# Performance work log

Hardware: AMD Instinct MI355X
Metric: run time of the kernel (lower is better)

## Reference

```python
import jax, jax.numpy as jnp
import numpy as np

B, N, F, H, MH = 8, 1024, 768, 12, 3072
DH = F // H
EPS = 1e-5

def _ln(x, g, b):
    mu = jnp.mean(x, axis=-1, keepdims=True)
    var = jnp.mean(jnp.square(x - mu), axis=-1, keepdims=True)
    return (x - mu) * jax.lax.rsqrt(var + EPS) * g + b

def setup_inputs() -> dict:
    key = jax.random.key(0)
    ks = jax.random.split(key, 16)
    s = 1.0 / np.sqrt(F)
    sm = 1.0 / np.sqrt(MH)
    return {
        "x": jax.random.normal(ks[0], (B, N, F), dtype=jnp.float32),
        "Wq": jax.random.uniform(ks[1], (F, F), jnp.float32, -s, s),
        "bq": jax.random.uniform(ks[2], (F,), jnp.float32, -s, s),
        "Wk": jax.random.uniform(ks[3], (F, F), jnp.float32, -s, s),
        "bk": jax.random.uniform(ks[4], (F,), jnp.float32, -s, s),
        "Wv": jax.random.uniform(ks[5], (F, F), jnp.float32, -s, s),
        "bv": jax.random.uniform(ks[6], (F,), jnp.float32, -s, s),
        "Wo": jax.random.uniform(ks[7], (F, F), jnp.float32, -s, s),
        "bo": jax.random.uniform(ks[8], (F,), jnp.float32, -s, s),
        "ln1_g": jnp.ones((F,), jnp.float32),
        "ln1_b": jnp.zeros((F,), jnp.float32),
        "ln2_g": jnp.ones((F,), jnp.float32),
        "ln2_b": jnp.zeros((F,), jnp.float32),
        "W1": jax.random.uniform(ks[9], (F, MH), jnp.float32, -s, s),
        "b1": jax.random.uniform(ks[10], (MH,), jnp.float32, -s, s),
        "W2": jax.random.uniform(ks[11], (MH, F), jnp.float32, -sm, sm),
        "b2": jax.random.uniform(ks[12], (F,), jnp.float32, -sm, sm),
    }

def reference(x, Wq, bq, Wk, bk, Wv, bv, Wo, bo, ln1_g, ln1_b, ln2_g, ln2_b, W1, b1, W2, b2):
    xn = _ln(x, ln1_g, ln1_b)
    # low-rank (here full-rank, rank=-1) QKV projections, split into heads -> [b,h,n,dh]
    q = (xn @ Wq + bq).reshape(B, N, H, DH).transpose(0, 2, 1, 3)
    k = (xn @ Wk + bk).reshape(B, N, H, DH).transpose(0, 2, 1, 3)
    v = (xn @ Wv + bv).reshape(B, N, H, DH).transpose(0, 2, 1, 3)
    # note: original scales by sqrt(feats), NOT sqrt(d_head)
    score = jax.nn.softmax(jnp.einsum('bhif,bhjf->bhij', q, k) / jnp.sqrt(jnp.float32(F)), axis=-1)
    attn = jnp.einsum('bhij,bhjf->bhif', score, v)
    attn = attn.transpose(0, 2, 1, 3).reshape(B, N, F)
    out = (attn @ Wo + bo) + x  # dropout p=0.0
    h = _ln(out, ln2_g, ln2_b)
    h = jax.nn.gelu(h @ W1 + b1, approximate=False)
    h = jax.nn.gelu(h @ W2 + b2, approximate=False)  # second GELU per source
    return h + out
```

## Files before the change

### kernel.cpp

```cpp
#include <hip/hip_runtime.h>
#include <math.h>

#define B_ 8
#define N_ 1024
#define F_ 768
#define H_ 12
#define DH_ 64
#define MH_ 3072
#define MROWS (B_ * N_)

typedef unsigned short u16;
typedef unsigned int u32;
typedef __bf16 bf16x8 __attribute__((ext_vector_type(8)));
typedef float f32x4 __attribute__((ext_vector_type(4)));

__device__ inline f32x4 mfma16(bf16x8 a, bf16x8 b, f32x4 c) {
  return __builtin_amdgcn_mfma_f32_16x16x32_bf16(a, b, c, 0, 0, 0);
}

__device__ inline u16 f2bu(float f) {
  u32 b = __builtin_bit_cast(u32, f);
  b += 0x7fffu + ((b >> 16) & 1u);
  return (u16)(b >> 16);
}
__device__ inline float bu2f(u16 u) {
  u32 x = ((u32)u) << 16;
  return __builtin_bit_cast(float, x);
}
__device__ inline float gelu_exact(float x) {
  return 0.5f * x * (1.0f + erff(x * 0.70710678118654752f));
}

#define AS1 __attribute__((address_space(1)))
#define AS3 __attribute__((address_space(3)))
__device__ inline void glds16(const void* g, void* l) {
  __builtin_amdgcn_global_load_lds((const AS1 void*)g, (AS3 void*)l, 16, 0, 0);
}

__device__ inline float ldf(const float* p) { return *p; }
__device__ inline float ldf(const u16* p) { return bu2f(*p); }

template <typename Tin>
__global__ __launch_bounds__(256) void transpose_bf16(
    const Tin* __restrict__ in, u16* __restrict__ out, int R, int C) {
  __shared__ float tile[64][65];
  size_t ibase = (size_t)blockIdx.z * (size_t)R * (size_t)C;
  size_t obase = (size_t)blockIdx.z * (size_t)R * (size_t)C;
  int r0 = blockIdx.y << 6, c0 = blockIdx.x << 6;
  int t = threadIdx.x;
#pragma unroll
  for (int i = 0; i < 16; ++i) {
    int idx = t + (i << 8);
    int r = idx >> 6, c = idx & 63;
    tile[r][c] = ldf(&in[ibase + (size_t)(r0 + r) * C + (c0 + c)]);
  }
  __syncthreads();
#pragma unroll
  for (int i = 0; i < 16; ++i) {
    int idx = t + (i << 8);
    int rr = idx >> 6, cc = idx & 63;
    out[obase + (size_t)(c0 + rr) * R + (r0 + cc)] = f2bu(tile[cc][rr]);
  }
}

__global__ __launch_bounds__(256) void concat_bias(
    const float* __restrict__ a, const float* __restrict__ b,
    const float* __restrict__ c, float* __restrict__ o) {
  int i = blockIdx.x * 256 + threadIdx.x;
  if (i < 768) o[i] = a[i];
  else if (i < 1536) o[i] = b[i - 768];
  else o[i] = c[i - 1536];
}

__global__ __launch_bounds__(256) void ln_to_bf16(
    const float* __restrict__ X, const float* __restrict__ gw,
    const float* __restrict__ bw, u16* __restrict__ Y) {
  int row = blockIdx.x;
  int t = threadIdx.x;
  const float* xr = X + (size_t)row * F_;
  float v0 = xr[t], v1 = xr[t + 256], v2 = xr[t + 512];
  float s = v0 + v1 + v2;
  float ss = v0 * v0 + v1 * v1 + v2 * v2;
#pragma unroll
  for (int off = 1; off < 64; off <<= 1) {
    s += __shfl_xor(s, off, 64);
    ss += __shfl_xor(ss, off, 64);
  }
  __shared__ float red[8];
  int wid = t >> 6, lane = t & 63;
  if (lane == 0) { red[wid] = s; red[4 + wid] = ss; }
  __syncthreads();
  s = red[0] + red[1] + red[2] + red[3];
  ss = red[4] + red[5] + red[6] + red[7];
  float mu = s * (1.0f / F_);
  float var = ss * (1.0f / F_) - mu * mu;
  float rstd = rsqrtf(var + 1e-5f);
  u16* yr = Y + (size_t)row * F_;
  yr[t] = f2bu((v0 - mu) * rstd * gw[t] + bw[t]);
  yr[t + 256] = f2bu((v1 - mu) * rstd * gw[t + 256] + bw[t + 256]);
  yr[t + 512] = f2bu((v2 - mu) * rstd * gw[t + 512] + bw[t + 512]);
}

template <int MODE>
__global__ __launch_bounds__(256) void gemm_bt(
    const u16* __restrict__ A, const u16* __restrict__ Bt,
    const float* __restrict__ bias, void* __restrict__ outp,
    const float* __restrict__ resid, int Ndim, int Kdim, float qscale) {
  __shared__ __attribute__((aligned(16))) u16 As[2][128][32];
  __shared__ __attribute__((aligned(16))) u16 Bs[2][128][32];
  int t = threadIdx.x;
  int lane = t & 63, wid = t >> 6;

  int nwg = gridDim.x;
  int q8 = nwg >> 3;
  int bid = blockIdx.x;
  int swz = (bid & 7) * q8 + (bid >> 3);
  int nnt = Ndim >> 7;
  int mt = swz / nnt, nt = swz - mt * nnt;
  int row0 = mt << 7, col0 = nt << 7;

  int wr = (wid >> 1) << 6, wc = (wid & 1) << 6;
  int lr = lane & 15, lk = (lane >> 4) << 3;
  int rbase = (lane >> 4) << 2;
  f32x4 zero = {0.f, 0.f, 0.f, 0.f};
  f32x4 acc[4][4];
#pragma unroll
  for (int m = 0; m < 4; ++m)
#pragma unroll
    for (int n = 0; n < 4; ++n) acc[m][n] = zero;

  int o0 = (wid << 10) + (lane << 4);
  int srow = o0 >> 6;
  int scol = (o0 & 63) >> 1;
  const u16* Ag = A + (size_t)(row0 + srow) * Kdim + scol;
  const u16* Bg = Bt + (size_t)(col0 + srow) * Kdim + scol;
  char* AsB = (char*)&As[0][0][0] + (wid << 10);
  char* BsB = (char*)&Bs[0][0][0] + (wid << 10);
  size_t half = (size_t)64 * Kdim;

  auto STAGE = [&](int buf, int kt) {
    int bo = buf << 13;
    glds16(Ag + kt, AsB + bo);
    glds16(Ag + kt + half, AsB + bo + 4096);
    glds16(Bg + kt, BsB + bo);
    glds16(Bg + kt + half, BsB + bo + 4096);
  };

  STAGE(0, 0);
  __syncthreads();
  int nk = Kdim >> 5;
  for (int ki = 0; ki < nk; ++ki) {
    int buf = ki & 1;
    if (ki + 1 < nk) STAGE(buf ^ 1, (ki + 1) << 5);
    bf16x8 af[4], bfr[4];
#pragma unroll
    for (int m = 0; m < 4; ++m) af[m] = *(const bf16x8*)&As[buf][wr + (m << 4) + lr][lk];
#pragma unroll
    for (int n = 0; n < 4; ++n) bfr[n] = *(const bf16x8*)&Bs[buf][wc + (n << 4) + lr][lk];
#pragma unroll
    for (int m = 0; m < 4; ++m)
#pragma unroll
      for (int n = 0; n < 4; ++n) acc[m][n] = mfma16(af[m], bfr[n], acc[m][n]);
    __syncthreads();
  }

#pragma unroll
  for (int n = 0; n < 4; ++n) {
    int col = col0 + wc + (n << 4) + lr;
    float bc = bias[col];
    int sub = 0, hh = 0, dh = 0;
    float sc = 1.0f;
    if constexpr (MODE == 0) {
      sub = (col >= 1536) ? 2 : (col >= 768 ? 1 : 0);
      int c = col - sub * 768;
      hh = c >> 6; dh = c & 63;
      sc = (sub == 0) ? qscale : 1.0f;
    }
#pragma unroll
    for (int m = 0; m < 4; ++m) {
#pragma unroll
      for (int r = 0; r < 4; ++r) {
        int row = row0 + wr + (m << 4) + rbase + r;
        float val = acc[m][n][r] + bc;
        if constexpr (MODE == 0) {
          int b = row >> 10, nn = row & 1023;
          ((u16*)outp)[(size_t)sub * 6291456 +
                       ((((size_t)b * H_ + hh) << 10) + nn) * DH_ + dh] = f2bu(val * sc);
        } else if constexpr (MODE == 1) {
          val += resid[(size_t)row * Ndim + col];
          ((float*)outp)[(size_t)row * Ndim + col] = val;
        } else if constexpr (MODE == 2) {
          ((u16*)outp)[(size_t)row * Ndim + col] = f2bu(gelu_exact(val));
        } else {
          val = gelu_exact(val) + resid[(size_t)row * Ndim + col];
          ((float*)outp)[(size_t)row * Ndim + col] = val;
        }
      }
    }
  }
}

__global__ __launch_bounds__(256, 3) void attn_fwd(
    const u16* __restrict__ Q, const u16* __restrict__ K,
    const u16* __restrict__ Vt, u16* __restrict__ Aout) {
  __shared__ __attribute__((aligned(16))) u16 Ks[64][72];
  __shared__ __attribute__((aligned(16))) u16 Vs[64][72];
  __shared__ __attribute__((aligned(16))) u16 Ps[4][32][72];
  int t = threadIdx.x, lane = t & 63, wid = t >> 6;

  int bid = blockIdx.x;
  int swz = (bid & 7) * 96 + (bid >> 3);
  int bh = swz >> 3;
  int qt = swz & 7;
  int q0 = (qt << 7) + (wid << 5);

  int lr = lane & 15, lk = (lane >> 4) << 3;
  int rbase = (lane >> 4) << 2;

  bf16x8 qf[2][2];
#pragma unroll
  for (int m = 0; m < 2; ++m)
#pragma unroll
    for (int ks = 0; ks < 2; ++ks)
      qf[m][ks] = *(const bf16x8*)&Q[((size_t)bh * N_ + q0 + (m << 4) + lr) * DH_ + (ks << 5) + lk];

  float lsum[2][4];
  f32x4 zero = {0.f, 0.f, 0.f, 0.f};
  f32x4 Oacc[2][4];
#pragma unroll
  for (int m = 0; m < 2; ++m) {
#pragma unroll
    for (int r = 0; r < 4; ++r) lsum[m][r] = 0.f;
#pragma unroll
    for (int nd = 0; nd < 4; ++nd) Oacc[m][nd] = zero;
  }

  int srow = t >> 3;
  int scol = (t & 7) << 3;
  const u16* Kg = K + ((size_t)bh * N_ + srow) * DH_ + scol;
  const u16* Vg = Vt + ((size_t)bh * DH_ + srow) * N_ + scol;

  for (int kt = 0; kt < 16; ++kt) {
    __syncthreads();
    *(uint4*)&Ks[srow][scol]      = *(const uint4*)(Kg + (size_t)(kt << 6) * DH_);
    *(uint4*)&Ks[srow + 32][scol] = *(const uint4*)(Kg + (size_t)((kt << 6) + 32) * DH_);
    *(uint4*)&Vs[srow][scol]      = *(const uint4*)(Vg + (kt << 6));
    *(uint4*)&Vs[srow + 32][scol] = *(const uint4*)(Vg + (size_t)32 * N_ + (kt << 6));
    __syncthreads();

    f32x4 s[2][4];
#pragma unroll
    for (int m = 0; m < 2; ++m)
#pragma unroll
      for (int n = 0; n < 4; ++n) s[m][n] = zero;
#pragma unroll
    for (int ks = 0; ks < 2; ++ks) {
      bf16x8 kf[4];
#pragma unroll
      for (int n = 0; n < 4; ++n) kf[n] = *(const bf16x8*)&Ks[(n << 4) + lr][(ks << 5) + lk];
#pragma unroll
      for (int m = 0; m < 2; ++m)
#pragma unroll
        for (int n = 0; n < 4; ++n) s[m][n] = mfma16(qf[m][ks], kf[n], s[m][n]);
    }

#pragma unroll
    for (int m = 0; m < 2; ++m)
#pragma unroll
      for (int n = 0; n < 4; ++n)
#pragma unroll
        for (int r = 0; r < 4; ++r) {
          float p = exp2f(s[m][n][r]);
          lsum[m][r] += p;
          Ps[wid][(m << 4) + rbase + r][(n << 4) + lr] = f2bu(p);
        }

#pragma unroll
    for (int ks = 0; ks < 2; ++ks) {
      bf16x8 pf[2], vf[4];
#pragma unroll
      for (int m = 0; m < 2; ++m) pf[m] = *(const bf16x8*)&Ps[wid][(m << 4) + lr][(ks << 5) + lk];
#pragma unroll
      for (int nd = 0; nd < 4; ++nd) vf[nd] = *(const bf16x8*)&Vs[(nd << 4) + lr][(ks << 5) + lk];
#pragma unroll
      for (int m = 0; m < 2; ++m)
#pragma unroll
        for (int nd = 0; nd < 4; ++nd) Oacc[m][nd] = mfma16(pf[m], vf[nd], Oacc[m][nd]);
    }
  }

  int b = bh / H_, h = bh % H_;
#pragma unroll
  for (int m = 0; m < 2; ++m)
#pragma unroll
    for (int r = 0; r < 4; ++r) {
      float sv = lsum[m][r];
#pragma unroll
      for (int off = 1; off < 16; off <<= 1) sv += __shfl_xor(sv, off, 64);
      float inv = 1.0f / sv;
      int row = q0 + (m << 4) + rbase + r;
      size_t orow = ((size_t)b * N_ + row) * F_ + (size_t)h * DH_;
#pragma unroll
      for (int nd = 0; nd < 4; ++nd)
        Aout[orow + (nd << 4) + lr] = f2bu(Oacc[m][nd][r] * inv);
    }
}

extern "C" void kernel_launch(void* const* d_in, const int* in_sizes, int n_in,
                              void* d_out, int out_size, void* d_ws, size_t ws_size,
                              hipStream_t stream) {
  (void)in_sizes; (void)n_in; (void)out_size; (void)ws_size;
  const float* x   = (const float*)d_in[0];
  const float* Wq  = (const float*)d_in[1];
  const float* bq  = (const float*)d_in[2];
  const float* Wk  = (const float*)d_in[3];
  const float* bk  = (const float*)d_in[4];
  const float* Wv  = (const float*)d_in[5];
  const float* bv  = (const float*)d_in[6];
  const float* Wo  = (const float*)d_in[7];
  const float* bo  = (const float*)d_in[8];
  const float* g1  = (const float*)d_in[9];
  const float* bn1 = (const float*)d_in[10];
  const float* g2  = (const float*)d_in[11];
  const float* bn2 = (const float*)d_in[12];
  const float* W1  = (const float*)d_in[13];
  const float* b1  = (const float*)d_in[14];
  const float* W2  = (const float*)d_in[15];
  const float* b2  = (const float*)d_in[16];

  char* ws = (char*)d_ws;
  size_t off = 0;
  auto alloc = [&](size_t bytes) {
    char* p = ws + off;
    off += (bytes + 255) & ~(size_t)255;
    return p;
  };
  u16* Wqkvt = (u16*)alloc((size_t)3 * F_ * F_ * 2);
  u16* Wot  = (u16*)alloc((size_t)F_ * F_ * 2);
  u16* W1t  = (u16*)alloc((size_t)MH_ * F_ * 2);
  u16* W2t  = (u16*)alloc((size_t)MH_ * F_ * 2);
  float* bqkv = (float*)alloc((size_t)3 * F_ * 4);
  u16* xn  = (u16*)alloc((size_t)MROWS * F_ * 2);
  u16* qb  = (u16*)alloc((size_t)B_ * H_ * N_ * DH_ * 2);
  u16* kb  = (u16*)alloc((size_t)B_ * H_ * N_ * DH_ * 2);
  u16* vb  = (u16*)alloc((size_t)B_ * H_ * N_ * DH_ * 2);
  u16* vt  = (u16*)alloc((size_t)B_ * H_ * N_ * DH_ * 2);
  u16* attn = (u16*)alloc((size_t)MROWS * F_ * 2);
  float* outb = (float*)alloc((size_t)MROWS * F_ * 4);
  u16* h1 = qb;
  u16* hn = xn;

  const float QSCALE = 0.052058773227f;

  dim3 blk(256);
  transpose_bf16<float><<<dim3(12, 12, 1), blk, 0, stream>>>(Wq, Wqkvt, F_, F_);
  transpose_bf16<float><<<dim3(12, 12, 1), blk, 0, stream>>>(Wk, Wqkvt + (size_t)F_ * F_, F_, F_);
  transpose_bf16<float><<<dim3(12, 12, 1), blk, 0, stream>>>(Wv, Wqkvt + (size_t)2 * F_ * F_, F_, F_);
  transpose_bf16<float><<<dim3(12, 12, 1), blk, 0, stream>>>(Wo, Wot, F_, F_);
  transpose_bf16<float><<<dim3(48, 12, 1), blk, 0, stream>>>(W1, W1t, F_, MH_);
  transpose_bf16<float><<<dim3(12, 48, 1), blk, 0, stream>>>(W2, W2t, MH_, F_);
  concat_bias<<<dim3(9), blk, 0, stream>>>(bq, bk, bv, bqkv);
  ln_to_bf16<<<dim3(MROWS), blk, 0, stream>>>(x, g1, bn1, xn);
  gemm_bt<0><<<dim3(18 * 64), blk, 0, stream>>>(xn, Wqkvt, bqkv, qb, nullptr, 3 * F_, F_, QSCALE);
  transpose_bf16<u16><<<dim3(1, 16, 96), blk, 0, stream>>>(vb, vt, N_, DH_);
  attn_fwd<<<dim3(768), blk, 0, stream>>>(qb, kb, vt, attn);
  gemm_bt<1><<<dim3(6 * 64), blk, 0, stream>>>(attn, Wot, bo, outb, x, F_, F_, 1.0f);
  ln_to_bf16<<<dim3(MROWS), blk, 0, stream>>>(outb, g2, bn2, hn);
  gemm_bt<2><<<dim3(24 * 64), blk, 0, stream>>>(hn, W1t, b1, h1, nullptr, MH_, F_, 1.0f);
  gemm_bt<3><<<dim3(6 * 64), blk, 0, stream>>>(h1, W2t, b2, d_out, outb, F_, MH_, 1.0f);
}
```

Measured before the change: 318.7 us.

## Triple-buffer GEMM staging with swizzled LDS and prefetch attention K/V tiles

The GEMM kernel moves from a double to a triple-buffered LDS pipeline. It uses explicit vmcnt waits and a single barrier per k-step, XOR-swizzles the LDS column layout to cut bank conflicts, and raises wave priority around the MFMA block. The attention kernel now loads the next K/V tile into registers while the current tile is being computed, hiding global-load latency. The cost is more LDS per GEMM block, which may reduce occupancy, plus hand-written waitcnt logic that must match the number of in-flight loads.

```diff
diff --git a/kernel.cpp b/kernel.cpp
--- a/kernel.cpp
+++ b/kernel.cpp
@@ -106,8 +106,8 @@
     const u16* __restrict__ A, const u16* __restrict__ Bt,
     const float* __restrict__ bias, void* __restrict__ outp,
     const float* __restrict__ resid, int Ndim, int Kdim, float qscale) {
-  __shared__ __attribute__((aligned(16))) u16 As[2][128][32];
-  __shared__ __attribute__((aligned(16))) u16 Bs[2][128][32];
+  __shared__ __attribute__((aligned(16))) u16 As[3][128][32];
+  __shared__ __attribute__((aligned(16))) u16 Bs[3][128][32];
   int t = threadIdx.x;
   int lane = t & 63, wid = t >> 6;
 
@@ -121,6 +121,7 @@
 
   int wr = (wid >> 1) << 6, wc = (wid & 1) << 6;
   int lr = lane & 15, lk = (lane >> 4) << 3;
+  int lkA = lk ^ ((lr & 3) << 3);
   int rbase = (lane >> 4) << 2;
   f32x4 zero = {0.f, 0.f, 0.f, 0.f};
   f32x4 acc[4][4];
@@ -129,39 +130,48 @@
 #pragma unroll
     for (int n = 0; n < 4; ++n) acc[m][n] = zero;
 
-  int o0 = (wid << 10) + (lane << 4);
-  int srow = o0 >> 6;
-  int scol = (o0 & 63) >> 1;
+  int srow = (wid << 4) + (lane >> 2);
+  int scol = ((lane & 3) << 3) ^ (((lane >> 2) & 3) << 3);
   const u16* Ag = A + (size_t)(row0 + srow) * Kdim + scol;
   const u16* Bg = Bt + (size_t)(col0 + srow) * Kdim + scol;
   char* AsB = (char*)&As[0][0][0] + (wid << 10);
   char* BsB = (char*)&Bs[0][0][0] + (wid << 10);
   size_t half = (size_t)64 * Kdim;
 
-  auto STAGE = [&](int buf, int kt) {
-    int bo = buf << 13;
+  auto STAGE = [&](int slot, int kt) {
+    int bo = slot << 13;
     glds16(Ag + kt, AsB + bo);
     glds16(Ag + kt + half, AsB + bo + 4096);
     glds16(Bg + kt, BsB + bo);
     glds16(Bg + kt + half, BsB + bo + 4096);
   };
 
+  int nk = Kdim >> 5;
   STAGE(0, 0);
-  __syncthreads();
-  int nk = Kdim >> 5;
-  for (int ki = 0; ki < nk; ++ki) {
-    int buf = ki & 1;
-    if (ki + 1 < nk) STAGE(buf ^ 1, (ki + 1) << 5);
+  if (nk > 1) STAGE(1, 32);
+  int sl0 = 0, sl1 = 1, sl2 = 2;
+  for (int i = 0; i < nk; ++i) {
+    if (i + 1 < nk) {
+      asm volatile("s_waitcnt vmcnt(4)" ::: "memory");
+    } else {
+      asm volatile("s_waitcnt vmcnt(0)" ::: "memory");
+    }
+    __builtin_amdgcn_sched_barrier(0);
+    __builtin_amdgcn_s_barrier();
+    __builtin_amdgcn_sched_barrier(0);
+    if (i + 2 < nk) STAGE(sl2, (i + 2) << 5);
     bf16x8 af[4], bfr[4];
 #pragma unroll
-    for (int m = 0; m < 4; ++m) af[m] = *(const bf16x8*)&As[buf][wr + (m << 4) + lr][lk];
-#pragma unroll
-    for (int n = 0; n < 4; ++n) bfr[n] = *(const bf16x8*)&Bs[buf][wc + (n << 4) + lr][lk];
+    for (int m = 0; m < 4; ++m) af[m] = *(const bf16x8*)&As[sl0][wr + (m << 4) + lr][lkA];
+#pragma unroll
+    for (int n = 0; n < 4; ++n) bfr[n] = *(const bf16x8*)&Bs[sl0][wc + (n << 4) + lr][lkA];
+    __builtin_amdgcn_s_setprio(1);
 #pragma unroll
     for (int m = 0; m < 4; ++m)
 #pragma unroll
       for (int n = 0; n < 4; ++n) acc[m][n] = mfma16(af[m], bfr[n], acc[m][n]);
-    __syncthreads();
+    __builtin_amdgcn_s_setprio(0);
+    int tmp = sl0; sl0 = sl1; sl1 = sl2; sl2 = tmp;
   }
 
 #pragma unroll
@@ -240,12 +250,22 @@
   const u16* Kg = K + ((size_t)bh * N_ + srow) * DH_ + scol;
   const u16* Vg = Vt + ((size_t)bh * DH_ + srow) * N_ + scol;
 
+  uint4 kr0, kr1, vr0, vr1;
+  auto LOADKV = [&](int kt) {
+    kr0 = *(const uint4*)(Kg + (size_t)(kt << 6) * DH_);
+    kr1 = *(const uint4*)(Kg + (size_t)((kt << 6) + 32) * DH_);
+    vr0 = *(const uint4*)(Vg + (kt << 6));
+    vr1 = *(const uint4*)(Vg + (size_t)32 * N_ + (kt << 6));
+  };
+  LOADKV(0);
+
   for (int kt = 0; kt < 16; ++kt) {
     __syncthreads();
-    *(uint4*)&Ks[srow][scol]      = *(const uint4*)(Kg + (size_t)(kt << 6) * DH_);
-    *(uint4*)&Ks[srow + 32][scol] = *(const uint4*)(Kg + (size_t)((kt << 6) + 32) * DH_);
-    *(uint4*)&Vs[srow][scol]      = *(const uint4*)(Vg + (kt << 6));
-    *(uint4*)&Vs[srow + 32][scol] = *(const uint4*)(Vg + (size_t)32 * N_ + (kt << 6));
+    *(uint4*)&Ks[srow][scol]      = kr0;
+    *(uint4*)&Ks[srow + 32][scol] = kr1;
+    *(uint4*)&Vs[srow][scol]      = vr0;
+    *(uint4*)&Vs[srow + 32][scol] = vr1;
+    if (kt + 1 < 16) LOADKV(kt + 1);
     __syncthreads();
 
     f32x4 s[2][4];
```

New measurement: 317.0 us. Within noise of the previous version (-0.5%).

## Use 256x128 GEMM tiles for QKV/FC1 and register-prefetch K/V in attention

Applied to the files above, without the earlier changes.

Adds a gemm_wide kernel that computes 256x128 output tiles per workgroup, with each wave holding an 8x4 accumulator block. It is used for the QKV projection and the first MLP GEMM to raise arithmetic intensity per LDS load and halve the grid. The cost is much higher register pressure and fewer waves per CU. The attention kernel also prefetches the next K/V tile into registers while the current tile is processed, to hide global load latency.

```diff
diff --git a/kernel.cpp b/kernel.cpp
--- a/kernel.cpp
+++ b/kernel.cpp
@@ -102,10 +102,103 @@
 }
 
 template <int MODE>
+__global__ __launch_bounds__(256, 2) void gemm_wide(
+    const u16* __restrict__ A, const u16* __restrict__ Bt,
+    const float* __restrict__ bias, void* __restrict__ outp,
+    int Ndim, int Kdim, float qscale) {
+  __shared__ __attribute__((aligned(16))) u16 As[2][256][32];
+  __shared__ __attribute__((aligned(16))) u16 Bs[2][128][32];
+  int t = threadIdx.x, lane = t & 63, wid = t >> 6;
+
+  int nwg = gridDim.x;
+  int q8 = nwg >> 3;
+  int bid = blockIdx.x;
+  int swz = (bid & 7) * q8 + (bid >> 3);
+  int nnt = Ndim >> 7;
+  int mt = swz / nnt, nt = swz - mt * nnt;
+  int row0 = mt << 8, col0 = nt << 7;
+
+  int wr2 = (wid >> 1) << 7;
+  int wc2 = (wid & 1) << 6;
+  int lr = lane & 15, lk = (lane >> 4) << 3;
+  int rbase = (lane >> 4) << 2;
+
+  f32x4 zero = {0.f, 0.f, 0.f, 0.f};
+  f32x4 acc[8][4];
+#pragma unroll
+  for (int m = 0; m < 8; ++m)
+#pragma unroll
+    for (int n = 0; n < 4; ++n) acc[m][n] = zero;
+
+  int srow = lane >> 2;
+  int scol = (lane & 3) << 3;
+  const u16* Ag = A + (size_t)(row0 + (wid << 6) + srow) * Kdim + scol;
+  const u16* Bg = Bt + (size_t)(col0 + (wid << 5) + srow) * Kdim + scol;
+  char* AsW = (char*)&As[0][0][0] + (wid << 12);
+  char* BsW = (char*)&Bs[0][0][0] + (wid << 11);
+
+  auto STAGE = [&](int buf, int kt) {
+#pragma unroll
+    for (int i = 0; i < 4; ++i)
+      glds16(Ag + (size_t)(i << 4) * Kdim + kt, AsW + (buf << 14) + (i << 10));
+#pragma unroll
+    for (int j = 0; j < 2; ++j)
+      glds16(Bg + (size_t)(j << 4) * Kdim + kt, BsW + (buf << 13) + (j << 10));
+  };
+
+  int nk = Kdim >> 5;
+  STAGE(0, 0);
+  __syncthreads();
+  for (int ki = 0; ki < nk; ++ki) {
+    int buf = ki & 1;
+    if (ki + 1 < nk) STAGE(buf ^ 1, (ki + 1) << 5);
+    bf16x8 af[8], bfr[4];
+#pragma unroll
+    for (int m = 0; m < 8; ++m) af[m] = *(const bf16x8*)&As[buf][wr2 + (m << 4) + lr][lk];
+#pragma unroll
+    for (int n = 0; n < 4; ++n) bfr[n] = *(const bf16x8*)&Bs[buf][wc2 + (n << 4) + lr][lk];
+#pragma unroll
+    for (int m = 0; m < 8; ++m)
+#pragma unroll
+      for (int n = 0; n < 4; ++n) acc[m][n] = mfma16(af[m], bfr[n], acc[m][n]);
+    __syncthreads();
+  }
+
+#pragma unroll
+  for (int n = 0; n < 4; ++n) {
+    int col = col0 + wc2 + (n << 4) + lr;
+    float bc = bias[col];
+    int sub = 0, hh = 0, dh = 0;
+    float sc = 1.0f;
+    if constexpr (MODE == 0) {
+      sub = (col >= 1536) ? 2 : (col >= 768 ? 1 : 0);
+      int c = col - sub * 768;
+      hh = c >> 6; dh = c & 63;
+      sc = (sub == 0) ? qscale : 1.0f;
+    }
+#pragma unroll
+    for (int m = 0; m < 8; ++m) {
+#pragma unroll
+      for (int r = 0; r < 4; ++r) {
+        int row = row0 + wr2 + (m << 4) + rbase + r;
+        float val = acc[m][n][r] + bc;
+        if constexpr (MODE == 0) {
+          int b = row >> 10, nn = row & 1023;
+          ((u16*)outp)[(size_t)sub * 6291456 +
+                       ((((size_t)b * H_ + hh) << 10) + nn) * DH_ + dh] = f2bu(val * sc);
+        } else {
+          ((u16*)outp)[(size_t)row * Ndim + col] = f2bu(gelu_exact(val));
+        }
+      }
+    }
+  }
+}
+
+template <int MODE>
 __global__ __launch_bounds__(256) void gemm_bt(
     const u16* __restrict__ A, const u16* __restrict__ Bt,
     const float* __restrict__ bias, void* __restrict__ outp,
-    const float* __restrict__ resid, int Ndim, int Kdim, float qscale) {
+    const float* __restrict__ resid, int Ndim, int Kdim) {
   __shared__ __attribute__((aligned(16))) u16 As[2][128][32];
   __shared__ __attribute__((aligned(16))) u16 Bs[2][128][32];
   int t = threadIdx.x;
@@ -168,29 +261,15 @@
   for (int n = 0; n < 4; ++n) {
     int col = col0 + wc + (n << 4) + lr;
     float bc = bias[col];
-    int sub = 0, hh = 0, dh = 0;
-    float sc = 1.0f;
-    if constexpr (MODE == 0) {
-      sub = (col >= 1536) ? 2 : (col >= 768 ? 1 : 0);
-      int c = col - sub * 768;
-      hh = c >> 6; dh = c & 63;
-      sc = (sub == 0) ? qscale : 1.0f;
-    }
 #pragma unroll
     for (int m = 0; m < 4; ++m) {
 #pragma unroll
       for (int r = 0; r < 4; ++r) {
         int row = row0 + wr + (m << 4) + rbase + r;
         float val = acc[m][n][r] + bc;
-        if constexpr (MODE == 0) {
-          int b = row >> 10, nn = row & 1023;
-          ((u16*)outp)[(size_t)sub * 6291456 +
-                       ((((size_t)b * H_ + hh) << 10) + nn) * DH_ + dh] = f2bu(val * sc);
-        } else if constexpr (MODE == 1) {
+        if constexpr (MODE == 1) {
           val += resid[(size_t)row * Ndim + col];
           ((float*)outp)[(size_t)row * Ndim + col] = val;
-        } else if constexpr (MODE == 2) {
-          ((u16*)outp)[(size_t)row * Ndim + col] = f2bu(gelu_exact(val));
         } else {
           val = gelu_exact(val) + resid[(size_t)row * Ndim + col];
           ((float*)outp)[(size_t)row * Ndim + col] = val;
@@ -240,12 +319,22 @@
   const u16* Kg = K + ((size_t)bh * N_ + srow) * DH_ + scol;
   const u16* Vg = Vt + ((size_t)bh * DH_ + srow) * N_ + scol;
 
+  uint4 kr0, kr1, vr0, vr1;
+  auto LOADKV = [&](int kt) {
+    kr0 = *(const uint4*)(Kg + (size_t)(kt << 6) * DH_);
+    kr1 = *(const uint4*)(Kg + (size_t)((kt << 6) + 32) * DH_);
+    vr0 = *(const uint4*)(Vg + (kt << 6));
+    vr1 = *(const uint4*)(Vg + (size_t)32 * N_ + (kt << 6));
+  };
+  LOADKV(0);
+
   for (int kt = 0; kt < 16; ++kt) {
     __syncthreads();
-    *(uint4*)&Ks[srow][scol]      = *(const uint4*)(Kg + (size_t)(kt << 6) * DH_);
-    *(uint4*)&Ks[srow + 32][scol] = *(const uint4*)(Kg + (size_t)((kt << 6) + 32) * DH_);
-    *(uint4*)&Vs[srow][scol]      = *(const uint4*)(Vg + (kt << 6));
-    *(uint4*)&Vs[srow + 32][scol] = *(const uint4*)(Vg + (size_t)32 * N_ + (kt << 6));
+    *(uint4*)&Ks[srow][scol]      = kr0;
+    *(uint4*)&Ks[srow + 32][scol] = kr1;
+    *(uint4*)&Vs[srow][scol]      = vr0;
+    *(uint4*)&Vs[srow + 32][scol] = vr1;
+    if (kt + 1 < 16) LOADKV(kt + 1);
     __syncthreads();
 
     f32x4 s[2][4];
@@ -361,11 +450,11 @@
   transpose_bf16<float><<<dim3(12, 48, 1), blk, 0, stream>>>(W2, W2t, MH_, F_);
   concat_bias<<<dim3(9), blk, 0, stream>>>(bq, bk, bv, bqkv);
   ln_to_bf16<<<dim3(MROWS), blk, 0, stream>>>(x, g1, bn1, xn);
-  gemm_bt<0><<<dim3(18 * 64), blk, 0, stream>>>(xn, Wqkvt, bqkv, qb, nullptr, 3 * F_, F_, QSCALE);
+  gemm_wide<0><<<dim3(32 * 18), blk, 0, stream>>>(xn, Wqkvt, bqkv, qb, 3 * F_, F_, QSCALE);
   transpose_bf16<u16><<<dim3(1, 16, 96), blk, 0, stream>>>(vb, vt, N_, DH_);
   attn_fwd<<<dim3(768), blk, 0, stream>>>(qb, kb, vt, attn);
-  gemm_bt<1><<<dim3(6 * 64), blk, 0, stream>>>(attn, Wot, bo, outb, x, F_, F_, 1.0f);
+  gemm_bt<1><<<dim3(6 * 64), blk, 0, stream>>>(attn, Wot, bo, outb, x, F_, F_);
   ln_to_bf16<<<dim3(MROWS), blk, 0, stream>>>(outb, g2, bn2, hn);
-  gemm_bt<2><<<dim3(24 * 64), blk, 0, stream>>>(hn, W1t, b1, h1, nullptr, MH_, F_, 1.0f);
-  gemm_bt<3><<<dim3(6 * 64), blk, 0, stream>>>(h1, W2t, b2, d_out, outb, F_, MH_, 1.0f);
-}
+  gemm_wide<2><<<dim3(32 * 24), blk, 0, stream>>>(hn, W1t, b1, h1, MH_, F_, 1.0f);
+  gemm_bt<3><<<dim3(6 * 64), blk, 0, stream>>>(h1, W2t, b2, d_out, outb, F_, MH_);
+}
```

Result: slower. 340.6 us (+6.9%).
